# Kernel tuning notes

Measured on AMD Instinct MI355X. Metric: run time of the kernel, lower is better.

The kernel has to match this reference:

```python
import jax, jax.numpy as jnp
import numpy as np

T_ITERS = 10
EPS = 1e-5


def setup_inputs() -> dict:
    key = jax.random.key(0)
    B, C, H, W = 64, 256, 56, 56
    X = jax.random.normal(key, (B, C, H, W), dtype=jnp.float32)
    # running_rot buffer: orthogonal rotation per group (g=1)
    M = np.random.default_rng(0).standard_normal((C, C)).astype(np.float32)
    q, _ = np.linalg.qr(M)
    running_rot = jnp.asarray(q[None, :, :])  # [g=1, d, d]
    return {"X": X, "running_rot": running_rot}


def _whiten(X, g, nc):
    # X: [B, C, H, W] -> x: [g, d, m] with m = B*H*W (training-mode IterNorm)
    B, C, H, W = X.shape
    x = jnp.transpose(X, (1, 0, 2, 3)).reshape(g, nc, -1)
    m = x.shape[-1]
    mean = jnp.mean(x, axis=-1, keepdims=True)          # [g, d, 1]
    xc = x - mean                                        # [g, d, m]
    I = jnp.broadcast_to(jnp.eye(nc, dtype=X.dtype), (g, nc, nc))
    Sigma = EPS * I + jnp.matmul(xc, jnp.swapaxes(xc, 1, 2)) * (1.0 / m)
    # rTr = 1 / trace(Sigma) per group
    rTr = 1.0 / jnp.sum(Sigma * I, axis=(1, 2), keepdims=True)  # [g,1,1]
    Sigma_N = Sigma * rTr
    # Newton-Schulz iteration: P_{k+1} = 1.5 P_k - 0.5 P_k^3 Sigma_N
    P = I
    for _ in range(T_ITERS):
        P3 = jnp.matmul(jnp.matmul(P, P), P)
        P = 1.5 * P - 0.5 * jnp.matmul(P3, Sigma_N)
    wm = P * jnp.sqrt(rTr)                               # whitening matrix [g,d,d]
    xn = jnp.matmul(wm, xc)                              # [g, d, m]
    return xn.reshape(C, B, H, W).transpose(1, 0, 2, 3)  # back to [B,C,H,W]


def reference(X, running_rot):
    g, _, nc = running_rot.shape
    B, C, H, W = X.shape
    X_hat = _whiten(X, g, nc)                            # [B, C, H, W]
    Xg = X_hat.reshape(B, g, nc, H, W)
    # rotate whitened features: Q^T alignment, einsum('bgchw,gdc->bgdhw')
    Xr = jnp.einsum('bgchw,gdc->bgdhw', Xg, running_rot)
    return Xr.reshape(B, C, H, W)
```

## Files before the change

kernel.cpp:

```cpp
#include <hip/hip_runtime.h>
#include <math.h>

#define HWn   3136
#define Cn    256
#define KCPB  49
#define NCHUNK 3136
#define INV_M (1.0f/200704.0f)
#define EPSc  1e-5f

typedef __attribute__((ext_vector_type(4))) float f32x4;
typedef __attribute__((ext_vector_type(8))) short s16x8;
typedef __attribute__((ext_vector_type(4))) unsigned short u16x4;

static __device__ __forceinline__ unsigned short f2bf(float f) {
  unsigned int u = __builtin_bit_cast(unsigned int, f);
  u = (u + 0x7fffu + ((u >> 16) & 1u)) >> 16;
  return (unsigned short)u;
}

static __device__ __forceinline__ unsigned int cvt_pk_bf16(float lo, float hi) {
  unsigned int r;
  asm("v_cvt_pk_bf16_f32 %0, %1, %2" : "=v"(r) : "v"(lo), "v"(hi));
  return r;
}

__global__ __launch_bounds__(1024) void k_gram(const float* __restrict__ X,
                                               float* __restrict__ Gp,
                                               float* __restrict__ Sp,
                                               int nparts) {
  __shared__ __align__(16) unsigned short lds[2][256 * 64];
  const int t = threadIdx.x, p = blockIdx.x;
  const int w = t >> 6, l = t & 63, a = l & 15, g = l >> 4;
  const int swzA = (a & 7) << 3;
  const int crow = t >> 4, sg = t & 15;

  f32x4 acc[16];
#pragma unroll
  for (int j = 0; j < 16; ++j) acc[j] = (f32x4){0.f, 0.f, 0.f, 0.f};
  float sum4[4] = {0.f, 0.f, 0.f, 0.f};
  float vx[16];

  const int start = (int)(((long)NCHUNK * p) / nparts);
  const int end   = (int)(((long)NCHUNK * (p + 1)) / nparts);

#define G_LOADS(CH)                                                           \
  {                                                                           \
    const int b_ = (CH) / KCPB, kc_ = (CH) % KCPB;                            \
    const float* xb_ = X + (long)b_ * Cn * HWn + kc_ * 64;                    \
    _Pragma("unroll")                                                         \
    for (int p4 = 0; p4 < 4; ++p4) {                                          \
      const float4 v = *(const float4*)(xb_ + (long)(p4 * 64 + crow) * HWn + sg * 4); \
      vx[p4 * 4 + 0] = v.x; vx[p4 * 4 + 1] = v.y;                             \
      vx[p4 * 4 + 2] = v.z; vx[p4 * 4 + 3] = v.w;                             \
    }                                                                         \
  }

#define G_CVTWR(BUF)                                                          \
  {                                                                           \
    _Pragma("unroll")                                                         \
    for (int p4 = 0; p4 < 4; ++p4) {                                          \
      const int c_ = p4 * 64 + crow;                                          \
      sum4[p4] += (vx[p4 * 4 + 0] + vx[p4 * 4 + 1])                           \
                + (vx[p4 * 4 + 2] + vx[p4 * 4 + 3]);                          \
      uint2 hh;                                                               \
      hh.x = cvt_pk_bf16(vx[p4 * 4 + 0], vx[p4 * 4 + 1]);                     \
      hh.y = cvt_pk_bf16(vx[p4 * 4 + 2], vx[p4 * 4 + 3]);                     \
      *(uint2*)(&lds[BUF][0] + ((c_ * 64 + sg * 4) ^ ((c_ & 7) << 3))) = hh;  \
    }                                                                         \
  }

  G_LOADS(start);
  G_CVTWR(0);
  __syncthreads();

  for (int ch = start; ch < end; ++ch) {
    const int cur = (ch - start) & 1;
    if (ch + 1 < end) G_LOADS(ch + 1);
    const unsigned short* tile = &lds[cur][0];
#pragma unroll
    for (int kk = 0; kk < 64; kk += 32) {
      const s16x8 fw = *(const s16x8*)(tile + (((w * 16 + a) * 64 + kk + g * 8) ^ swzA));
#pragma unroll
      for (int j = 0; j < 16; ++j) {
        const s16x8 fj = *(const s16x8*)(tile + (((j * 16 + a) * 64 + kk + g * 8) ^ swzA));
        acc[j] = __builtin_amdgcn_mfma_f32_16x16x32_bf16(fw, fj, acc[j], 0, 0, 0);
      }
    }
    if (ch + 1 < end) G_CVTWR(cur ^ 1);
    __syncthreads();
  }
#undef G_LOADS
#undef G_CVTWR

  float* gout = Gp + (long)p * 65536;
#pragma unroll
  for (int j = 0; j < 16; ++j)
#pragma unroll
    for (int r = 0; r < 4; ++r)
      gout[(16 * w + 4 * g + r) * 256 + 16 * j + a] = acc[j][r];

#pragma unroll
  for (int p4 = 0; p4 < 4; ++p4) {
    float s = sum4[p4];
    s += __shfl_xor(s, 1);
    s += __shfl_xor(s, 2);
    s += __shfl_xor(s, 4);
    s += __shfl_xor(s, 8);
    if (a == 0) Sp[(long)p * 256 + p4 * 64 + w * 4 + g] = s;
  }
}

__global__ __launch_bounds__(1024) void k_reduce(const float* __restrict__ Gp,
                                                 const float* __restrict__ Sp,
                                                 float* __restrict__ Sigma,
                                                 float* __restrict__ diag,
                                                 float* __restrict__ meansum,
                                                 int nparts) {
  __shared__ float redA[4][256];
  __shared__ float msh[256];
  __shared__ __align__(16) float redB[16][256];
  const int t = threadIdx.x, j = blockIdx.x;
  const int c = t & 255, g = t >> 8;

  {
    float s = 0.f;
    const int pa0 = (nparts * g) >> 2, pa1 = (nparts * (g + 1)) >> 2;
    for (int p = pa0; p < pa1; ++p) s += Sp[(long)p * 256 + c];
    redA[g][c] = s;
  }
  __syncthreads();
  if (g == 0) msh[c] = (redA[0][c] + redA[1][c]) + (redA[2][c] + redA[3][c]);

  {
    const int c4 = (t & 63) * 4, sl = t >> 6;
    const int pb0 = (nparts * sl) >> 4, pb1 = (nparts * (sl + 1)) >> 4;
    const float* gp = Gp + (long)pb0 * 65536 + (long)j * 256 + c4;
    f32x4 s4 = (f32x4){0.f, 0.f, 0.f, 0.f};
    for (int p = pb0; p < pb1; ++p) { s4 += *(const f32x4*)gp; gp += 65536; }
    *(f32x4*)&redB[sl][c4] = s4;
  }
  __syncthreads();

  if (t < 256) {
    float t0 = 0.f, t1 = 0.f;
#pragma unroll
    for (int sl = 0; sl < 16; sl += 2) { t0 += redB[sl][t]; t1 += redB[sl + 1][t]; }
    const float tot = t0 + t1;
    const float mc = msh[t] * INV_M;
    const float mj = msh[j] * INV_M;
    const float sig = tot * INV_M - mj * mc + ((j == t) ? EPSc : 0.f);
    Sigma[(long)j * 256 + t] = sig;
    if (t == j) diag[j] = sig;
    if (j == 0) meansum[t] = msh[t];
  }
}

__global__ __launch_bounds__(1024) void k_it0(const float* __restrict__ Sig,
                                              const float* __restrict__ diag,
                                              float* __restrict__ P1,
                                              float* __restrict__ scal) {
  __shared__ float trs[256];
  const int t = threadIdx.x, c = t & 255, kh = t >> 8;
  const int row = blockIdx.x * 4 + kh;
  if (t < 256) trs[t] = diag[t];
  __syncthreads();
  for (int st = 128; st > 0; st >>= 1) {
    if (t < st) trs[t] += trs[t + st];
    __syncthreads();
  }
  const float tr = trs[0];
  const float rTr = 1.0f / tr;
  P1[(long)row * 256 + c] = ((row == c) ? 1.5f : 0.f) - 0.5f * rTr * Sig[(long)row * 256 + c];
  if (blockIdx.x == 0 && t == 0) {
    scal[0] = tr;
    scal[1] = rTr;
    scal[2] = sqrtf(rTr);
  }
}

__global__ __launch_bounds__(1024) void k_ns(const float* __restrict__ Ps,
                                             float* __restrict__ Pd,
                                             const float* __restrict__ Sig,
                                             const float* __restrict__ scal) {
  __shared__ __align__(16) float PT[256][4];
  __shared__ __align__(16) float red[4][256][4];
  const int t = threadIdx.x, c = t & 255, kh = t >> 8, k0 = kh * 64;
  const int r0 = blockIdx.x * 4;

  PT[c][kh] = Ps[(r0 + kh) * 256 + c];
  __syncthreads();

  f32x4 acc;

#define NS_PHASE(BPTR)                                                        \
  {                                                                           \
    acc = (f32x4){0.f, 0.f, 0.f, 0.f};                                        \
    const float* Bb = (BPTR) + (long)k0 * 256 + c;                            \
    _Pragma("unroll 8")                                                       \
    for (int kk = 0; kk < 64; ++kk) {                                         \
      const float b = Bb[(long)kk * 256];                                     \
      const f32x4 a4 = *(const f32x4*)&PT[k0 + kk][0];                        \
      acc += a4 * b;                                                          \
    }                                                                         \
    *(f32x4*)&red[kh][c][0] = acc;                                            \
    __syncthreads();                                                          \
  }

#define NS_COMBINE()                                                          \
  {                                                                           \
    const f32x4 vs = (*(const f32x4*)&red[0][c][0] + *(const f32x4*)&red[1][c][0]) \
                   + (*(const f32x4*)&red[2][c][0] + *(const f32x4*)&red[3][c][0]); \
    if (kh == 0) *(f32x4*)&PT[c][0] = vs;                                     \
    __syncthreads();                                                          \
  }

  NS_PHASE(Ps);
  NS_COMBINE();
  NS_PHASE(Ps);
  NS_COMBINE();
  NS_PHASE(Sig);

  const float rTr = scal[1];
  const float t3 = ((red[0][c][kh] + red[1][c][kh]) + (red[2][c][kh] + red[3][c][kh]));
  const float pr = Ps[(r0 + kh) * 256 + c];
  Pd[(r0 + kh) * 256 + c] = 1.5f * pr - 0.5f * rTr * t3;
#undef NS_PHASE
#undef NS_COMBINE
}

__global__ void k_makeA(const float* __restrict__ rot, const float* __restrict__ P,
                        const float* __restrict__ scal, const float* __restrict__ meansum,
                        unsigned short* __restrict__ Abf, float* __restrict__ bias) {
  __shared__ float Rw[8][256];
  __shared__ float Tw[8][256];
  const int r0 = blockIdx.x * 8, c = threadIdx.x;
#pragma unroll
  for (int r = 0; r < 8; ++r) Rw[r][c] = rot[(r0 + r) * 256 + c];
  __syncthreads();
  float t[8];
#pragma unroll
  for (int r = 0; r < 8; ++r) t[r] = 0.f;
  for (int k = 0; k < 256; ++k) {
    const float pv = P[k * 256 + c];
#pragma unroll
    for (int r = 0; r < 8; ++r) t[r] += Rw[r][k] * pv;
  }
  const float s = scal[2];
  const float mc = meansum[c] * INV_M;
#pragma unroll
  for (int r = 0; r < 8; ++r) {
    const float av = t[r] * s;
    Abf[(r0 + r) * 256 + c] = f2bf(av);
    Tw[r][c] = av * mc;
  }
  __syncthreads();
  for (int st = 128; st > 0; st >>= 1) {
    if (c < st) {
#pragma unroll
      for (int r = 0; r < 8; ++r) Tw[r][c] += Tw[r][c + st];
    }
    __syncthreads();
  }
  if (c == 0) {
#pragma unroll
    for (int r = 0; r < 8; ++r) bias[r0 + r] = Tw[r][0];
  }
}

__global__ __launch_bounds__(1024) void k_apply(const float* __restrict__ X,
                                                const unsigned short* __restrict__ Abf,
                                                const float* __restrict__ bias,
                                                float* __restrict__ out) {
  __shared__ __align__(16) unsigned short lds[2][64 * 256];
  const int t = threadIdx.x, w = t >> 6, l = t & 63, a = l & 15, g = l >> 4;
  const int bid = blockIdx.x;
  const int b = bid >> 3, strip = bid & 7;
  const int ch0 = (49 * strip) >> 3, ch1 = (49 * (strip + 1)) >> 3;

  const int d = 16 * w + a;
  s16x8 af[8];
#pragma unroll
  for (int kk8 = 0; kk8 < 8; ++kk8)
    af[kk8] = *(const s16x8*)(Abf + d * 256 + kk8 * 32 + g * 8);
  const float bd = bias[d];

  const float* xbase = X + (long)b * Cn * HWn;
  float* obase = out + (long)b * Cn * HWn;
  float vx[16];

#define A_LOADS(CH)                                                           \
  {                                                                           \
    const int s0_ = (CH) * 64;                                                \
    _Pragma("unroll")                                                         \
    for (int p4 = 0; p4 < 4; ++p4) {                                          \
      const int c4_ = p4 * 16 + w;                                            \
      const float* xp_ = xbase + (long)(c4_ * 4) * HWn + s0_ + l;             \
      vx[p4 * 4 + 0] = xp_[0];                                                \
      vx[p4 * 4 + 1] = xp_[HWn];                                              \
      vx[p4 * 4 + 2] = xp_[2 * HWn];                                          \
      vx[p4 * 4 + 3] = xp_[3 * HWn];                                          \
    }                                                                         \
  }

#define A_CVTWR(BUF)                                                          \
  {                                                                           \
    _Pragma("unroll")                                                         \
    for (int p4 = 0; p4 < 4; ++p4) {                                          \
      const int c4_ = p4 * 16 + w;                                            \
      uint2 hh;                                                               \
      hh.x = cvt_pk_bf16(vx[p4 * 4 + 0], vx[p4 * 4 + 1]);                     \
      hh.y = cvt_pk_bf16(vx[p4 * 4 + 2], vx[p4 * 4 + 3]);                     \
      *(uint2*)(&lds[BUF][0] + ((l * 256 + c4_ * 4) ^ ((l & 7) << 3))) = hh;  \
    }                                                                         \
  }

  A_LOADS(ch0);
  A_CVTWR(0);
  __syncthreads();

  for (int ch = ch0; ch < ch1; ++ch) {
    const int cur = (ch - ch0) & 1;
    if (ch + 1 < ch1) A_LOADS(ch + 1);

    const unsigned short* tile = &lds[cur][0];
    f32x4 acc[4];
#pragma unroll
    for (int st = 0; st < 4; ++st) acc[st] = (f32x4){0.f, 0.f, 0.f, 0.f};
#pragma unroll
    for (int kk8 = 0; kk8 < 8; ++kk8) {
#pragma unroll
      for (int st = 0; st < 4; ++st) {
        const s16x8 xf = *(const s16x8*)(tile + (((st * 16 + a) * 256 + kk8 * 32 + g * 8) ^ ((a & 7) << 3)));
        acc[st] = __builtin_amdgcn_mfma_f32_16x16x32_bf16(xf, af[kk8], acc[st], 0, 0, 0);
      }
    }
    const int s0 = ch * 64;
#pragma unroll
    for (int st = 0; st < 4; ++st) {
      const f32x4 o = acc[st] - bd;
      __builtin_nontemporal_store(o, (f32x4*)(obase + (long)d * HWn + s0 + st * 16 + 4 * g));
    }

    if (ch + 1 < ch1) A_CVTWR(cur ^ 1);
    __syncthreads();
  }
#undef A_LOADS
#undef A_CVTWR
}

extern "C" void kernel_launch(void* const* d_in, const int* in_sizes, int n_in,
                              void* d_out, int out_size, void* d_ws, size_t ws_size,
                              hipStream_t stream) {
  const float* X = (const float*)d_in[0];
  const float* rot = (const float*)d_in[1];
  float* out = (float*)d_out;

  auto need = [](int np) -> size_t {
    return (size_t)4 * ((size_t)np * 65536 + (size_t)np * 256 + 3 * 65536
                        + 256 + 256 + 16 + 256)
         + (size_t)2 * 65536;
  };
  int nparts = 128;
  while (nparts > 4 && need(nparts) > ws_size) nparts >>= 1;

  float* w = (float*)d_ws;
  float* Gp = w;       w += (size_t)nparts * 65536;
  float* Sp = w;       w += (size_t)nparts * 256;
  float* Sigma = w;    w += 65536;
  float* P0 = w;       w += 65536;
  float* P1 = w;       w += 65536;
  float* diag = w;     w += 256;
  float* meansum = w;  w += 256;
  float* scal = w;     w += 16;
  float* bias = w;     w += 256;
  unsigned short* Abf = (unsigned short*)w;

  k_gram<<<dim3(nparts), dim3(1024), 0, stream>>>(X, Gp, Sp, nparts);
  k_reduce<<<dim3(256), dim3(1024), 0, stream>>>(Gp, Sp, Sigma, diag, meansum, nparts);
  k_it0<<<dim3(64), dim3(1024), 0, stream>>>(Sigma, diag, P1, scal);
  float* ps = P1;
  float* pd = P0;
  for (int i = 0; i < 9; ++i) {
    k_ns<<<dim3(64), dim3(1024), 0, stream>>>(ps, pd, Sigma, scal);
    float* tmp = ps; ps = pd; pd = tmp;
  }
  k_makeA<<<dim3(32), dim3(256), 0, stream>>>(rot, ps, scal, meansum, Abf, bias);
  k_apply<<<dim3(512), dim3(1024), 0, stream>>>(X, Abf, bias, out);
}
```

Baseline: 297.6 us.

## Fold trace into reduce and fuse last Newton-Schulz step with rotation matrix build

```diff
diff --git a/kernel.cpp b/kernel.cpp
--- a/kernel.cpp
+++ b/kernel.cpp
@@ -27,6 +27,7 @@
 __global__ __launch_bounds__(1024) void k_gram(const float* __restrict__ X,
                                                float* __restrict__ Gp,
                                                float* __restrict__ Sp,
+                                               float* __restrict__ Dp,
                                                int nparts) {
   __shared__ __align__(16) unsigned short lds[2][256 * 64];
   const int t = threadIdx.x, p = blockIdx.x;
@@ -97,7 +98,8 @@
   for (int j = 0; j < 16; ++j)
 #pragma unroll
     for (int r = 0; r < 4; ++r)
-      gout[(16 * w + 4 * g + r) * 256 + 16 * j + a] = acc[j][r];
+      __builtin_nontemporal_store(acc[j][r],
+          gout + (16 * w + 4 * g + r) * 256 + 16 * j + a);
 
 #pragma unroll
   for (int p4 = 0; p4 < 4; ++p4) {
@@ -108,16 +110,43 @@
     s += __shfl_xor(s, 8);
     if (a == 0) Sp[(long)p * 256 + p4 * 64 + w * 4 + g] = s;
   }
+
+  {
+    float dsum = 0.f;
+#pragma unroll
+    for (int j = 0; j < 16; ++j) {
+      if (j == w && (a >> 2) == g) {
+#pragma unroll
+        for (int r = 0; r < 4; ++r)
+          if ((a & 3) == r) dsum = acc[j][r];
+      }
+    }
+#pragma unroll
+    for (int off = 1; off < 64; off <<= 1) dsum += __shfl_xor(dsum, off);
+    float* lf = (float*)lds;
+    if (l == 0) lf[w] = dsum;
+    __syncthreads();
+    if (t == 0) {
+      float d = 0.f;
+#pragma unroll
+      for (int ww = 0; ww < 16; ++ww) d += lf[ww];
+      Dp[p] = d;
+    }
+  }
 }
 
 __global__ __launch_bounds__(1024) void k_reduce(const float* __restrict__ Gp,
                                                  const float* __restrict__ Sp,
+                                                 const float* __restrict__ Dp,
                                                  float* __restrict__ Sigma,
-                                                 float* __restrict__ diag,
+                                                 float* __restrict__ P1,
                                                  float* __restrict__ meansum,
+                                                 float* __restrict__ scal,
                                                  int nparts) {
   __shared__ float redA[4][256];
   __shared__ float msh[256];
+  __shared__ float scrD[256];
+  __shared__ float scrM[256];
   __shared__ __align__(16) float redB[16][256];
   const int t = threadIdx.x, j = blockIdx.x;
   const int c = t & 255, g = t >> 8;
@@ -130,13 +159,30 @@
   }
   __syncthreads();
   if (g == 0) msh[c] = (redA[0][c] + redA[1][c]) + (redA[2][c] + redA[3][c]);
+  __syncthreads();
+
+  if (t < 256) {
+    scrD[t] = (t < nparts) ? Dp[t] : 0.f;
+    const float mc = msh[t] * INV_M;
+    scrM[t] = mc * mc;
+  }
+  __syncthreads();
+  for (int st = 128; st > 0; st >>= 1) {
+    if (t < st) { scrD[t] += scrD[t + st]; scrM[t] += scrM[t + st]; }
+    __syncthreads();
+  }
+  const float tr = scrD[0] * INV_M - scrM[0] + 256.f * EPSc;
+  const float rTr = 1.0f / tr;
 
   {
     const int c4 = (t & 63) * 4, sl = t >> 6;
     const int pb0 = (nparts * sl) >> 4, pb1 = (nparts * (sl + 1)) >> 4;
     const float* gp = Gp + (long)pb0 * 65536 + (long)j * 256 + c4;
     f32x4 s4 = (f32x4){0.f, 0.f, 0.f, 0.f};
-    for (int p = pb0; p < pb1; ++p) { s4 += *(const f32x4*)gp; gp += 65536; }
+    for (int p = pb0; p < pb1; ++p) {
+      s4 += __builtin_nontemporal_load((const f32x4*)gp);
+      gp += 65536;
+    }
     *(f32x4*)&redB[sl][c4] = s4;
   }
   __syncthreads();
@@ -150,31 +196,11 @@
     const float mj = msh[j] * INV_M;
     const float sig = tot * INV_M - mj * mc + ((j == t) ? EPSc : 0.f);
     Sigma[(long)j * 256 + t] = sig;
-    if (t == j) diag[j] = sig;
-    if (j == 0) meansum[t] = msh[t];
-  }
-}
-
-__global__ __launch_bounds__(1024) void k_it0(const float* __restrict__ Sig,
-                                              const float* __restrict__ diag,
-                                              float* __restrict__ P1,
-                                              float* __restrict__ scal) {
-  __shared__ float trs[256];
-  const int t = threadIdx.x, c = t & 255, kh = t >> 8;
-  const int row = blockIdx.x * 4 + kh;
-  if (t < 256) trs[t] = diag[t];
-  __syncthreads();
-  for (int st = 128; st > 0; st >>= 1) {
-    if (t < st) trs[t] += trs[t + st];
-    __syncthreads();
-  }
-  const float tr = trs[0];
-  const float rTr = 1.0f / tr;
-  P1[(long)row * 256 + c] = ((row == c) ? 1.5f : 0.f) - 0.5f * rTr * Sig[(long)row * 256 + c];
-  if (blockIdx.x == 0 && t == 0) {
-    scal[0] = tr;
-    scal[1] = rTr;
-    scal[2] = sqrtf(rTr);
+    P1[(long)j * 256 + t] = ((j == t) ? 1.5f : 0.f) - 0.5f * rTr * sig;
+    if (j == 0) {
+      meansum[t] = msh[t];
+      if (t == 0) { scal[0] = tr; scal[1] = rTr; scal[2] = sqrtf(rTr); }
+    }
   }
 }
 
@@ -224,47 +250,50 @@
   const float t3 = ((red[0][c][kh] + red[1][c][kh]) + (red[2][c][kh] + red[3][c][kh]));
   const float pr = Ps[(r0 + kh) * 256 + c];
   Pd[(r0 + kh) * 256 + c] = 1.5f * pr - 0.5f * rTr * t3;
+}
+
+__global__ __launch_bounds__(1024) void k_ns_makeA(const float* __restrict__ Ps,
+                                                   const float* __restrict__ Sig,
+                                                   const float* __restrict__ rot,
+                                                   const float* __restrict__ scal,
+                                                   const float* __restrict__ meansum,
+                                                   unsigned short* __restrict__ Abf,
+                                                   float* __restrict__ bias) {
+  __shared__ __align__(16) float PT[256][4];
+  __shared__ __align__(16) float red[4][256][4];
+  __shared__ float Tw[4][256];
+  const int t = threadIdx.x, c = t & 255, kh = t >> 8, k0 = kh * 64;
+  const int r0 = blockIdx.x * 4;
+
+  PT[c][kh] = rot[(r0 + kh) * 256 + c];
+  __syncthreads();
+
+  f32x4 acc;
+
+  NS_PHASE(Ps);
+  NS_COMBINE();
+  const float t1 = PT[c][kh];
+  NS_PHASE(Ps);
+  NS_COMBINE();
+  NS_PHASE(Ps);
+  NS_COMBINE();
+  NS_PHASE(Sig);
+
+  const float rTr = scal[1];
+  const float sq = scal[2];
+  const float t4 = (red[0][c][kh] + red[1][c][kh]) + (red[2][c][kh] + red[3][c][kh]);
+  const float av = sq * (1.5f * t1 - 0.5f * rTr * t4);
+  Abf[(r0 + kh) * 256 + c] = f2bf(av);
+  const float mc = meansum[c] * INV_M;
+  Tw[kh][c] = av * mc;
+  __syncthreads();
+  for (int st = 128; st > 0; st >>= 1) {
+    if (c < st) Tw[kh][c] += Tw[kh][c + st];
+    __syncthreads();
+  }
+  if (c == 0) bias[r0 + kh] = Tw[kh][0];
 #undef NS_PHASE
 #undef NS_COMBINE
-}
-
-__global__ void k_makeA(const float* __restrict__ rot, const float* __restrict__ P,
-                        const float* __restrict__ scal, const float* __restrict__ meansum,
-                        unsigned short* __restrict__ Abf, float* __restrict__ bias) {
-  __shared__ float Rw[8][256];
-  __shared__ float Tw[8][256];
-  const int r0 = blockIdx.x * 8, c = threadIdx.x;
-#pragma unroll
-  for (int r = 0; r < 8; ++r) Rw[r][c] = rot[(r0 + r) * 256 + c];
-  __syncthreads();
-  float t[8];
-#pragma unroll
-  for (int r = 0; r < 8; ++r) t[r] = 0.f;
-  for (int k = 0; k < 256; ++k) {
-    const float pv = P[k * 256 + c];
-#pragma unroll
-    for (int r = 0; r < 8; ++r) t[r] += Rw[r][k] * pv;
-  }
-  const float s = scal[2];
-  const float mc = meansum[c] * INV_M;
-#pragma unroll
-  for (int r = 0; r < 8; ++r) {
-    const float av = t[r] * s;
-    Abf[(r0 + r) * 256 + c] = f2bf(av);
-    Tw[r][c] = av * mc;
-  }
-  __syncthreads();
-  for (int st = 128; st > 0; st >>= 1) {
-    if (c < st) {
-#pragma unroll
-      for (int r = 0; r < 8; ++r) Tw[r][c] += Tw[r][c + st];
-    }
-    __syncthreads();
-  }
-  if (c == 0) {
-#pragma unroll
-    for (int r = 0; r < 8; ++r) bias[r0 + r] = Tw[r][0];
-  }
 }
 
 __global__ __launch_bounds__(1024) void k_apply(const float* __restrict__ X,
@@ -356,8 +385,8 @@
   float* out = (float*)d_out;
 
   auto need = [](int np) -> size_t {
-    return (size_t)4 * ((size_t)np * 65536 + (size_t)np * 256 + 3 * 65536
-                        + 256 + 256 + 16 + 256)
+    return (size_t)4 * ((size_t)np * 65536 + (size_t)np * 256 + (size_t)np
+                        + 3 * 65536 + 256 + 16 + 256)
          + (size_t)2 * 65536;
   };
   int nparts = 128;
@@ -366,24 +395,23 @@
   float* w = (float*)d_ws;
   float* Gp = w;       w += (size_t)nparts * 65536;
   float* Sp = w;       w += (size_t)nparts * 256;
+  float* Dp = w;       w += (size_t)nparts;
   float* Sigma = w;    w += 65536;
   float* P0 = w;       w += 65536;
   float* P1 = w;       w += 65536;
-  float* diag = w;     w += 256;
   float* meansum = w;  w += 256;
   float* scal = w;     w += 16;
   float* bias = w;     w += 256;
   unsigned short* Abf = (unsigned short*)w;
 
-  k_gram<<<dim3(nparts), dim3(1024), 0, stream>>>(X, Gp, Sp, nparts);
-  k_reduce<<<dim3(256), dim3(1024), 0, stream>>>(Gp, Sp, Sigma, diag, meansum, nparts);
-  k_it0<<<dim3(64), dim3(1024), 0, stream>>>(Sigma, diag, P1, scal);
+  k_gram<<<dim3(nparts), dim3(1024), 0, stream>>>(X, Gp, Sp, Dp, nparts);
+  k_reduce<<<dim3(256), dim3(1024), 0, stream>>>(Gp, Sp, Dp, Sigma, P1, meansum, scal, nparts);
   float* ps = P1;
   float* pd = P0;
-  for (int i = 0; i < 9; ++i) {
+  for (int i = 0; i < 8; ++i) {
     k_ns<<<dim3(64), dim3(1024), 0, stream>>>(ps, pd, Sigma, scal);
     float* tmp = ps; ps = pd; pd = tmp;
   }
-  k_makeA<<<dim3(32), dim3(256), 0, stream>>>(rot, ps, scal, meansum, Abf, bias);
+  k_ns_makeA<<<dim3(64), dim3(1024), 0, stream>>>(ps, Sigma, rot, scal, meansum, Abf, bias);
   k_apply<<<dim3(512), dim3(1024), 0, stream>>>(X, Abf, bias, out);
 }
```

After: 285.0 us. 1.04x faster.
